# Kernel tuning notes

Hardware: AMD Instinct MI355X
Metric: run time of the kernel (lower is better)

Reference implementation:

```python
import jax, jax.numpy as jnp
import numpy as np

H = 256   # node_hidden_dim == edge_hidden_dim

def _ln(x, g, b):
    m = x.mean(-1, keepdims=True)
    v = ((x - m) ** 2).mean(-1, keepdims=True)
    return (x - m) / jnp.sqrt(v + 1e-5) * g + b

def _slnn(x, W, b, g, beta):
    # Linear -> LayerNorm -> ReLU (SingleLayerNN)
    return jax.nn.relu(_ln(x @ W.T + b, g, beta))

def _gru_mean(x, Wih, Whh, bih, bhh):
    # x: [E, T, Din]; torch GRU gate order (r, z, n); returns mean over time of outputs [E, H]
    h0 = jnp.zeros((x.shape[0], Whh.shape[1]), x.dtype)
    def step(h, xt):
        gi = xt @ Wih.T + bih
        gh = h @ Whh.T + bhh
        ir, iz, inn = jnp.split(gi, 3, axis=-1)
        hr, hz, hn = jnp.split(gh, 3, axis=-1)
        r = jax.nn.sigmoid(ir + hr)
        z = jax.nn.sigmoid(iz + hz)
        n = jnp.tanh(inn + r * hn)
        h_new = (1.0 - z) * n + z * h
        return h_new, h_new
    _, ys = jax.lax.scan(step, h0, jnp.swapaxes(x, 0, 1))  # [T, E, H]
    return ys.mean(axis=0)

def setup_inputs() -> dict:
    key = jax.random.key(0)
    ks = iter(jax.random.split(key, 64))
    rn = lambda shape, s=1.0: (jax.random.normal(next(ks), shape, jnp.float32) * s)
    ru = lambda shape: jax.random.uniform(next(ks), shape, jnp.float32)
    ri = lambda shape, hi: jax.random.randint(next(ks), shape, 0, hi, jnp.int32)
    N0, N1, N2, E0, E1, T = 40000, 10000, 2000, 100000, 20000, 8
    Dn, De, FC, C = 128, 64, 512, 16
    inp = {
        'node_features': rn((N0, Dn)),
        'edge_features_0': rn((E0, T, De)),
        'edge_features_1': rn((E1, T, H)),
        'history_0': rn((N0, H)),
        'history_1': rn((N1, H)),
        'agg_history_1': rn((N2, H)),
        'subg_norm_1': ru((N1, 1)),
        'subg_norm_2': ru((N2, 1)),
        'norm_2': ru((N2, 1)),
        'src0': ri((E0,), N0), 'dst0': ri((E0,), N1),
        'src1': ri((E1,), N1), 'dst1': ri((E1,), N2),
        'self_nid0': ri((N1,), N0), 'self_nid1': ri((N2,), N1),
        # parameters
        'gru0_Wih': rn((3 * H, De), 0.05), 'gru0_Whh': rn((3 * H, H), 0.05),
        'gru0_bih': rn((3 * H,), 0.05), 'gru0_bhh': rn((3 * H,), 0.05),
        'gru1_Wih': rn((3 * H, H), 0.05), 'gru1_Whh': rn((3 * H, H), 0.05),
        'gru1_bih': rn((3 * H,), 0.05), 'gru1_bhh': rn((3 * H,), 0.05),
        'phi0_W': rn((H, Dn + H), 0.05), 'phi0_b': rn((H,), 0.05),
        'phi0_g': jnp.ones((H,)), 'phi0_beta': jnp.zeros((H,)),
        'phi1_W': rn((H, 2 * H), 0.05), 'phi1_b': rn((H,), 0.05),
        'phi1_g': jnp.ones((H,)), 'phi1_beta': jnp.zeros((H,)),
        'nu0_W': rn((H, 2 * H), 0.05), 'nu0_b': rn((H,), 0.05),
        'nu0_g': jnp.ones((H,)), 'nu0_beta': jnp.zeros((H,)),
        'nu1_W': rn((H, 2 * H), 0.05), 'nu1_b': rn((H,), 0.05),
        'nu1_g': jnp.ones((H,)), 'nu1_beta': jnp.zeros((H,)),
        'fc1_W': rn((FC, H), 0.05), 'fc1_b': rn((FC,), 0.05),
        'fc2_W': rn((C, FC), 0.05), 'fc2_b': rn((C,), 0.05),
    }
    return inp

def reference(node_features, edge_features_0, edge_features_1, history_0, history_1,
              agg_history_1, subg_norm_1, subg_norm_2, norm_2,
              gru0_Wih, gru0_Whh, gru0_bih, gru0_bhh,
              gru1_Wih, gru1_Whh, gru1_bih, gru1_bhh,
              phi0_W, phi0_b, phi0_g, phi0_beta,
              phi1_W, phi1_b, phi1_g, phi1_beta,
              nu0_W, nu0_b, nu0_g, nu0_beta,
              nu1_W, nu1_b, nu1_g, nu1_beta,
              fc1_W, fc1_b, fc2_W, fc2_b,
              src0, dst0, src1, dst1, self_nid0, self_nid1):
    N1, N2 = self_nid0.shape[0], self_nid1.shape[0]
    # ---- layer 0 ----
    self_h0 = _slnn(jnp.concatenate([jnp.zeros((N1, H), node_features.dtype),
                                     node_features[self_nid0]], 1),
                    phi0_W, phi0_b, phi0_g, phi0_beta)                       # [N1, H]
    edge_emb0 = _gru_mean(edge_features_0, gru0_Wih, gru0_Whh, gru0_bih, gru0_bhh)  # [E0, H]
    nb0 = _slnn(jnp.concatenate([node_features[src0], edge_emb0], 1),
                phi0_W, phi0_b, phi0_g, phi0_beta)
    msg0 = jax.nn.relu(nb0 - history_0[src0])
    delta_nb0 = jax.ops.segment_sum(msg0, dst0, num_segments=N1)             # scatter-sum
    new_h0 = (delta_nb0 - self_h0) * subg_norm_1
    h1 = _slnn(jnp.concatenate([new_h0, self_h0], 1), nu0_W, nu0_b, nu0_g, nu0_beta)  # [N1, H]
    # ---- layer 1 ----
    self_h1 = _slnn(jnp.concatenate([jnp.zeros((N2, H), h1.dtype), h1[self_nid1]], 1),
                    phi1_W, phi1_b, phi1_g, phi1_beta)                       # [N2, H]
    self_delta_h1 = self_h1 - history_1[self_nid1]
    edge_emb1 = _gru_mean(edge_features_1, gru1_Wih, gru1_Whh, gru1_bih, gru1_bhh)  # [E1, H]
    nb1 = _slnn(jnp.concatenate([h1[src1], edge_emb1], 1),
                phi1_W, phi1_b, phi1_g, phi1_beta)
    msg1 = jax.nn.relu(nb1 - history_1[src1])
    delta_nb1 = jax.ops.segment_sum(msg1, dst1, num_segments=N2)
    new_h1 = (delta_nb1 - self_delta_h1) * subg_norm_2 + agg_history_1 * norm_2
    h2 = _slnn(jnp.concatenate([new_h1, self_h1], 1), nu1_W, nu1_b, nu1_g, nu1_beta)  # [N2, H]
    # ---- readout (no activation between fc1 and fc2, as in source) ----
    logit = (h2 @ fc1_W.T + fc1_b) @ fc2_W.T + fc2_b
    return logit
```

## Files before the change

kernel.cpp:

```cpp
#include <hip/hip_runtime.h>

typedef unsigned short u16;
typedef __attribute__((ext_vector_type(4))) float f32x4;
typedef __attribute__((ext_vector_type(8))) short bf16x8;
#define MFMA16(a,b,c) __builtin_amdgcn_mfma_f32_16x16x32_bf16((a),(b),(c),0,0,0)

template<int N> struct ic { static constexpr int v = N; };

__device__ __forceinline__ u16 f2bf(float f){
  unsigned int u = __float_as_uint(f);
  u += 0x7FFFu + ((u >> 16) & 1u);
  return (u16)(u >> 16);
}
__device__ __forceinline__ float bf2f(u16 h){
  return __uint_as_float(((unsigned int)h) << 16);
}
__device__ __forceinline__ float sigmoid_f(float x){
  x = fminf(fmaxf(x, -30.f), 30.f);
  return __fdividef(1.f, 1.f + __expf(-x));
}
__device__ __forceinline__ float tanh_f(float x){
  x = fminf(fmaxf(x, -15.f), 15.f);
  float e = __expf(-2.f * x);
  return __fdividef(1.f - e, 1.f + e);
}

__global__ void cvt_bf16_kernel(const float* __restrict__ in, u16* __restrict__ out, int n){
  int i = blockIdx.x * 256 + threadIdx.x;
  int stride = gridDim.x * 256;
  for (; i < n; i += stride) out[i] = f2bf(in[i]);
}

template<int R>
__device__ __forceinline__ void ln_stats_rows(const float* __restrict__ O,
                                              float* __restrict__ mean_s,
                                              float* __restrict__ rstd_s){
  const int tid  = threadIdx.x;
  const int wave = tid >> 6, lane = tid & 63;
  constexpr int RW = R / 4;
  #pragma unroll
  for (int rr = 0; rr < RW; rr++){
    const int r = wave * RW + rr;
    float s = 0.f, q = 0.f;
    #pragma unroll
    for (int i = lane; i < 256; i += 64){ float v = O[r*256 + i]; s += v; q += v*v; }
    #pragma unroll
    for (int off = 32; off; off >>= 1){ s += __shfl_down(s, off); q += __shfl_down(q, off); }
    if (lane == 0){
      float m   = s * (1.f/256.f);
      float var = q * (1.f/256.f) - m*m;
      mean_s[r] = m;
      rstd_s[r] = rsqrtf(fmaxf(var, 0.f) + 1e-5f);
    }
  }
}

template<int DIN, int NFD>
__global__ __launch_bounds__(512, 2)
void gru_mfma_kernel(int E,
    const float* __restrict__ x,
    const float* __restrict__ nodef,
    const int*   __restrict__ src,
    const int*   __restrict__ dst,
    const float* __restrict__ hist,
    const u16*   __restrict__ Wih,
    const u16*   __restrict__ Whh,
    const float* __restrict__ bih,
    const float* __restrict__ bhh,
    const u16*   __restrict__ phiW,
    const float* __restrict__ phib,
    const float* __restrict__ phig,
    const float* __restrict__ phibeta,
    float* __restrict__ delta)
{
  constexpr int HP  = 264;
  constexpr int XP  = DIN + 8;
  constexpr int NP  = NFD + 8;
  constexpr int KP  = NFD + 256;
  constexpr int NF4 = DIN / 32;

  __shared__ u16  hb[2 * 64 * HP];
  __shared__ u16  xb[2 * 64 * XP];
  __shared__ float sums_s[8 * 64], sqs_s[8 * 64];
  __shared__ float mean_s[64], rstd_s[64];
  __shared__ int   srcs_s[64], dsts_s[64];

  const int tid  = threadIdx.x;
  const int wave = tid >> 6, lane = tid & 63;
  const int quad = lane >> 4, ln15 = lane & 15;
  const int cbase = wave * 32;
  const int e0   = blockIdx.x * 64;

  if (tid < 64){
    int e  = e0 + tid;
    int ec = (e < E) ? e : (E - 1);
    srcs_s[tid] = src[ec];
    dsts_s[tid] = dst[ec];
  }

  int cn[2]; float brc[2], bzc[2], bnic[2], bnhc[2], pb[2], gg[2], gb[2];
  #pragma unroll
  for (int nt = 0; nt < 2; nt++){
    int c   = cbase + nt * 16 + ln15;
    cn[nt]  = c;
    brc[nt]  = bih[c]       + bhh[c];
    bzc[nt]  = bih[256 + c] + bhh[256 + c];
    bnic[nt] = bih[512 + c];
    bnhc[nt] = bhh[512 + c];
    pb[nt]   = phib[c];
    gg[nt]   = phig[c];
    gb[nt]   = phibeta[c];
  }

  #pragma unroll
  for (int j = 0; j < NF4; j++){
    int i4 = tid + j * 512;
    int e  = i4 / (DIN / 4);
    int k4 = (i4 % (DIN / 4)) * 4;
    int ge = (e0 + e < E) ? (e0 + e) : (E - 1);
    float4 v = *(const float4*)(x + (size_t)ge * (8 * DIN) + k4);
    ushort4 u;
    u.x = f2bf(v.x); u.y = f2bf(v.y); u.z = f2bf(v.z); u.w = f2bf(v.w);
    *(ushort4*)(xb + e * XP + k4) = u;
  }
  __syncthreads();

  float hs[2][4][4];
  #pragma unroll
  for (int nt = 0; nt < 2; nt++)
    #pragma unroll
    for (int mt = 0; mt < 4; mt++)
      #pragma unroll
      for (int q = 0; q < 4; q++) hs[nt][mt][q] = 0.f;

  const f32x4 zero4 = {0.f, 0.f, 0.f, 0.f};

  #pragma unroll 1
  for (int t = 0; t < 8; t++){
    const u16* rd = hb + ((t & 1) ^ 1) * (64 * HP);
    u16*       wr = hb + (t & 1) * (64 * HP);
    const u16* xr = xb + (t & 1) * (64 * XP);

    float4 xpre[NF4];
    if (t < 7){
      #pragma unroll
      for (int j = 0; j < NF4; j++){
        int i4 = tid + j * 512;
        int e  = i4 / (DIN / 4);
        int k4 = (i4 % (DIN / 4)) * 4;
        int ge = (e0 + e < E) ? (e0 + e) : (E - 1);
        xpre[j] = *(const float4*)(x + (size_t)ge * (8 * DIN) + (size_t)(t + 1) * DIN + k4);
      }
    }

    auto phase = [&](auto ntc){
      constexpr int NT = decltype(ntc)::v;
      const int c = cn[NT];
      f32x4 aR[4], aZ[4], aNI[4], aNH[4];
      #pragma unroll
      for (int mt = 0; mt < 4; mt++){
        aR[mt] = zero4; aZ[mt] = zero4; aNI[mt] = zero4; aNH[mt] = zero4;
      }
      if (t > 0){
        #pragma unroll
        for (int kt = 0; kt < 8; kt++){
          bf16x8 a[4];
          #pragma unroll
          for (int mt = 0; mt < 4; mt++)
            a[mt] = *(const bf16x8*)(rd + (mt*16 + ln15) * HP + kt * 32 + quad * 8);
          const u16* bp = Whh + (size_t)c * 256 + kt * 32 + quad * 8;
          bf16x8 br = *(const bf16x8*)(bp);
          bf16x8 bz = *(const bf16x8*)(bp + 256 * 256);
          bf16x8 bn = *(const bf16x8*)(bp + 512 * 256);
          #pragma unroll
          for (int mt = 0; mt < 4; mt++){
            aR[mt]  = MFMA16(a[mt], br, aR[mt]);
            aZ[mt]  = MFMA16(a[mt], bz, aZ[mt]);
            aNH[mt] = MFMA16(a[mt], bn, aNH[mt]);
          }
        }
      }
      #pragma unroll
      for (int kt = 0; kt < DIN / 32; kt++){
        bf16x8 a[4];
        #pragma unroll
        for (int mt = 0; mt < 4; mt++)
          a[mt] = *(const bf16x8*)(xr + (mt*16 + ln15) * XP + kt * 32 + quad * 8);
        const u16* bp = Wih + (size_t)c * DIN + kt * 32 + quad * 8;
        bf16x8 br = *(const bf16x8*)(bp);
        bf16x8 bz = *(const bf16x8*)(bp + 256 * DIN);
        bf16x8 bn = *(const bf16x8*)(bp + 512 * DIN);
        #pragma unroll
        for (int mt = 0; mt < 4; mt++){
          aR[mt]  = MFMA16(a[mt], br, aR[mt]);
          aZ[mt]  = MFMA16(a[mt], bz, aZ[mt]);
          aNI[mt] = MFMA16(a[mt], bn, aNI[mt]);
        }
      }
      #pragma unroll
      for (int mt = 0; mt < 4; mt++){
        #pragma unroll
        for (int q = 0; q < 4; q++){
          const int e = mt * 16 + quad * 4 + q;
          float r = sigmoid_f(aR[mt][q] + brc[NT]);
          float z = sigmoid_f(aZ[mt][q] + bzc[NT]);
          float n = tanh_f(aNI[mt][q] + bnic[NT] + r * (aNH[mt][q] + bnhc[NT]));
          float hold = (t > 0) ? bf2f(rd[e * HP + c]) : 0.f;
          float hnew = (1.f - z) * n + z * hold;
          hs[NT][mt][q] += hnew;
          if (t < 7) wr[e * HP + c] = f2bf(hnew);
        }
      }
    };
    phase(ic<0>());
    phase(ic<1>());

    if (t < 7){
      u16* xw = xb + ((t + 1) & 1) * (64 * XP);
      #pragma unroll
      for (int j = 0; j < NF4; j++){
        int i4 = tid + j * 512;
        int e  = i4 / (DIN / 4);
        int k4 = (i4 % (DIN / 4)) * 4;
        ushort4 u;
        u.x = f2bf(xpre[j].x); u.y = f2bf(xpre[j].y);
        u.z = f2bf(xpre[j].z); u.w = f2bf(xpre[j].w);
        *(ushort4*)(xw + e * XP + k4) = u;
      }
    }
    __syncthreads();
  }

  {
    u16* eb = hb;
    #pragma unroll
    for (int nt = 0; nt < 2; nt++)
      #pragma unroll
      for (int mt = 0; mt < 4; mt++)
        #pragma unroll
        for (int q = 0; q < 4; q++){
          const int e = mt * 16 + quad * 4 + q;
          eb[e * HP + cn[nt]] = f2bf(hs[nt][mt][q] * 0.125f);
        }
    constexpr int R4 = NFD / 4;
    for (int i = tid; i < 64 * R4; i += 512){
      int e  = i / R4;
      int k4 = (i - e * R4) * 4;
      const float4 v = *(const float4*)(nodef + (size_t)srcs_s[e] * NFD + k4);
      ushort4 u;
      u.x = f2bf(v.x); u.y = f2bf(v.y); u.z = f2bf(v.z); u.w = f2bf(v.w);
      *(ushort4*)(xb + e * NP + k4) = u;
    }
  }
  __syncthreads();

  f32x4 P[2][4];
  #pragma unroll
  for (int nt = 0; nt < 2; nt++)
    #pragma unroll
    for (int mt = 0; mt < 4; mt++) P[nt][mt] = zero4;

  #pragma unroll
  for (int kt = 0; kt < NFD / 32; kt++){
    bf16x8 a[4];
    #pragma unroll
    for (int mt = 0; mt < 4; mt++)
      a[mt] = *(const bf16x8*)(xb + (mt*16 + ln15) * NP + kt * 32 + quad * 8);
    #pragma unroll
    for (int nt = 0; nt < 2; nt++){
      const u16* bp = phiW + (size_t)cn[nt] * KP + kt * 32 + quad * 8;
      bf16x8 b = *(const bf16x8*)(bp);
      #pragma unroll
      for (int mt = 0; mt < 4; mt++) P[nt][mt] = MFMA16(a[mt], b, P[nt][mt]);
    }
  }
  #pragma unroll
  for (int kt = 0; kt < 8; kt++){
    bf16x8 a[4];
    #pragma unroll
    for (int mt = 0; mt < 4; mt++)
      a[mt] = *(const bf16x8*)(hb + (mt*16 + ln15) * HP + kt * 32 + quad * 8);
    #pragma unroll
    for (int nt = 0; nt < 2; nt++){
      const u16* bp = phiW + (size_t)cn[nt] * KP + NFD + kt * 32 + quad * 8;
      bf16x8 b = *(const bf16x8*)(bp);
      #pragma unroll
      for (int mt = 0; mt < 4; mt++) P[nt][mt] = MFMA16(a[mt], b, P[nt][mt]);
    }
  }

  float sl[4][4], sq_[4][4];
  #pragma unroll
  for (int mt = 0; mt < 4; mt++)
    #pragma unroll
    for (int q = 0; q < 4; q++){
      float v0 = P[0][mt][q] + pb[0];
      float v1 = P[1][mt][q] + pb[1];
      P[0][mt][q] = v0; P[1][mt][q] = v1;
      sl[mt][q]  = v0 + v1;
      sq_[mt][q] = v0 * v0 + v1 * v1;
    }
  #pragma unroll
  for (int off = 1; off < 16; off <<= 1){
    #pragma unroll
    for (int mt = 0; mt < 4; mt++)
      #pragma unroll
      for (int q = 0; q < 4; q++){
        sl[mt][q]  += __shfl_xor(sl[mt][q], off);
        sq_[mt][q] += __shfl_xor(sq_[mt][q], off);
      }
  }
  if (ln15 == 0){
    #pragma unroll
    for (int mt = 0; mt < 4; mt++)
      #pragma unroll
      for (int q = 0; q < 4; q++){
        int row = mt * 16 + quad * 4 + q;
        sums_s[wave * 64 + row] = sl[mt][q];
        sqs_s[wave * 64 + row]  = sq_[mt][q];
      }
  }
  __syncthreads();
  if (tid < 64){
    float m = 0.f, qq = 0.f;
    #pragma unroll
    for (int w = 0; w < 8; w++){ m += sums_s[w * 64 + tid]; qq += sqs_s[w * 64 + tid]; }
    m  *= (1.f / 256.f);
    qq *= (1.f / 256.f);
    mean_s[tid] = m;
    rstd_s[tid] = rsqrtf(fmaxf(qq - m * m, 0.f) + 1e-5f);
  }
  __syncthreads();

  #pragma unroll
  for (int nt = 0; nt < 2; nt++){
    const int c = cn[nt];
    #pragma unroll
    for (int mt = 0; mt < 4; mt++)
      #pragma unroll
      for (int q = 0; q < 4; q++){
        const int e  = mt * 16 + quad * 4 + q;
        const int ge = e0 + e;
        float y = (P[nt][mt][q] - mean_s[e]) * rstd_s[e] * gg[nt] + gb[nt];
        y = fmaxf(y, 0.f);
        float mv = y - hist[(size_t)srcs_s[e] * 256 + c];
        if (ge < E && mv > 0.f)
          atomicAdd(delta + (size_t)dsts_s[e] * 256 + c, mv);
      }
  }
}

template<int K, int WS>
__global__ __launch_bounds__(256)
void self_slnn_kernel(int N,
    const float* __restrict__ feat,
    const int*   __restrict__ nid,
    const float* __restrict__ W,
    const float* __restrict__ b,
    const float* __restrict__ g,
    const float* __restrict__ beta,
    const float* __restrict__ hist,
    float* __restrict__ out,
    float* __restrict__ out2)
{
  constexpr int R = 8;
  __shared__ float X[R*K];
  __shared__ float O[R*256];
  __shared__ float mean_s[R], rstd_s[R];
  __shared__ int   nids[R];
  const int tid = threadIdx.x;
  const int n0  = blockIdx.x * R;
  if (tid < R) nids[tid] = (n0 + tid < N) ? nid[n0 + tid] : 0;
  __syncthreads();
  for (int i = tid; i < R*K; i += 256){
    int r = i / K, k = i - r*K;
    X[i] = feat[(size_t)nids[r]*K + k];
  }
  __syncthreads();
  const int c = tid;
  const float* Wc = W + (size_t)c*WS + (WS - K);
  float acc[R];
  const float bc0 = b[c];
  #pragma unroll
  for (int r = 0; r < R; r++) acc[r] = bc0;
  #pragma unroll 1
  for (int k = 0; k < K; k += 4){
    float4 w = *(const float4*)(Wc + k);
    #pragma unroll
    for (int r = 0; r < R; r++){
      float4 xv = *(const float4*)(X + r*K + k);
      acc[r] += w.x*xv.x + w.y*xv.y + w.z*xv.z + w.w*xv.w;
    }
  }
  #pragma unroll
  for (int r = 0; r < R; r++) O[r*256 + c] = acc[r];
  __syncthreads();
  ln_stats_rows<R>(O, mean_s, rstd_s);
  __syncthreads();
  const float gc = g[c], bc = beta[c];
  #pragma unroll
  for (int r = 0; r < R; r++){
    int n = n0 + r;
    if (n < N){
      float y = fmaxf((acc[r] - mean_s[r]) * rstd_s[r] * gc + bc, 0.f);
      out[(size_t)n*256 + c] = y;
      if (out2) out2[(size_t)n*256 + c] = y - hist[(size_t)nids[r]*256 + c];
    }
  }
}

__global__ __launch_bounds__(256)
void compose_slnn_kernel(int N,
    const float* __restrict__ delta,
    const float* __restrict__ selfA,
    const float* __restrict__ selfB,
    const float* __restrict__ subg,
    const float* __restrict__ agg,
    const float* __restrict__ normv,
    const float* __restrict__ W,
    const float* __restrict__ b,
    const float* __restrict__ g,
    const float* __restrict__ beta,
    float* __restrict__ out)
{
  constexpr int R = 8;
  __shared__ float X[R*512];
  __shared__ float O[R*256];
  __shared__ float mean_s[R], rstd_s[R];
  const int tid = threadIdx.x;
  const int n0  = blockIdx.x * R;
  for (int i = tid; i < R*512; i += 256){
    int r = i >> 9, k = i & 511;
    int n = n0 + r;
    float v = 0.f;
    if (n < N){
      if (k < 256){
        v = (delta[(size_t)n*256 + k] - selfA[(size_t)n*256 + k]) * subg[n];
        if (agg) v += agg[(size_t)n*256 + k] * normv[n];
      } else {
        v = selfB[(size_t)n*256 + (k - 256)];
      }
    }
    X[i] = v;
  }
  __syncthreads();
  const int c = tid;
  const float* Wc = W + (size_t)c*512;
  float acc[R];
  const float bc0 = b[c];
  #pragma unroll
  for (int r = 0; r < R; r++) acc[r] = bc0;
  #pragma unroll 1
  for (int k = 0; k < 512; k += 4){
    float4 w = *(const float4*)(Wc + k);
    #pragma unroll
    for (int r = 0; r < R; r++){
      float4 xv = *(const float4*)(X + r*512 + k);
      acc[r] += w.x*xv.x + w.y*xv.y + w.z*xv.z + w.w*xv.w;
    }
  }
  #pragma unroll
  for (int r = 0; r < R; r++) O[r*256 + c] = acc[r];
  __syncthreads();
  ln_stats_rows<R>(O, mean_s, rstd_s);
  __syncthreads();
  const float gc = g[c], bc = beta[c];
  #pragma unroll
  for (int r = 0; r < R; r++){
    int n = n0 + r;
    if (n < N)
      out[(size_t)n*256 + c] = fmaxf((acc[r] - mean_s[r]) * rstd_s[r] * gc + bc, 0.f);
  }
}

__global__ __launch_bounds__(256)
void readout_kernel(int N,
    const float* __restrict__ h2,
    const float* __restrict__ W1,
    const float* __restrict__ b1,
    const float* __restrict__ W2,
    const float* __restrict__ b2,
    float* __restrict__ out)
{
  constexpr int R = 8;
  __shared__ float X[R*256];
  __shared__ float T[R*512];
  const int tid = threadIdx.x;
  const int n0  = blockIdx.x * R;
  for (int i = tid; i < R*256; i += 256){
    int r = i >> 8, k = i & 255;
    int n = n0 + r;
    X[i] = (n < N) ? h2[(size_t)n*256 + k] : 0.f;
  }
  __syncthreads();
  const int c = tid;
  const float* Wa = W1 + (size_t)c*256;
  const float* Wb = W1 + (size_t)(c+256)*256;
  float acca[R], accb[R];
  const float ba = b1[c], bb = b1[c+256];
  #pragma unroll
  for (int r = 0; r < R; r++){ acca[r] = ba; accb[r] = bb; }
  #pragma unroll 1
  for (int k = 0; k < 256; k += 4){
    float4 wa = *(const float4*)(Wa + k);
    float4 wb = *(const float4*)(Wb + k);
    #pragma unroll
    for (int r = 0; r < R; r++){
      float4 xv = *(const float4*)(X + r*256 + k);
      acca[r] += wa.x*xv.x + wa.y*xv.y + wa.z*xv.z + wa.w*xv.w;
      accb[r] += wb.x*xv.x + wb.y*xv.y + wb.z*xv.z + wb.w*xv.w;
    }
  }
  #pragma unroll
  for (int r = 0; r < R; r++){ T[r*512 + c] = acca[r]; T[r*512 + 256 + c] = accb[r]; }
  __syncthreads();
  if (tid < R*16){
    int r = tid >> 4, o = tid & 15;
    int n = n0 + r;
    if (n < N){
      float s = b2[o];
      const float* w  = W2 + (size_t)o*512;
      const float* tr = T + r*512;
      #pragma unroll 4
      for (int k = 0; k < 512; k++) s += tr[k]*w[k];
      out[(size_t)n*16 + o] = s;
    }
  }
}

extern "C" void kernel_launch(void* const* d_in, const int* in_sizes, int n_in,
                              void* d_out, int out_size, void* d_ws, size_t ws_size,
                              hipStream_t stream) {
  const float* nf     = (const float*)d_in[0];
  const float* x0     = (const float*)d_in[1];
  const float* x1     = (const float*)d_in[2];
  const float* hist0  = (const float*)d_in[3];
  const float* hist1  = (const float*)d_in[4];
  const float* aggh1  = (const float*)d_in[5];
  const float* subg1  = (const float*)d_in[6];
  const float* subg2  = (const float*)d_in[7];
  const float* norm2  = (const float*)d_in[8];
  const int*   src0   = (const int*)d_in[9];
  const int*   dst0   = (const int*)d_in[10];
  const int*   src1   = (const int*)d_in[11];
  const int*   dst1   = (const int*)d_in[12];
  const int*   nid0   = (const int*)d_in[13];
  const int*   nid1   = (const int*)d_in[14];
  const float* g0Wih  = (const float*)d_in[15];
  const float* g0Whh  = (const float*)d_in[16];
  const float* g0bih  = (const float*)d_in[17];
  const float* g0bhh  = (const float*)d_in[18];
  const float* g1Wih  = (const float*)d_in[19];
  const float* g1Whh  = (const float*)d_in[20];
  const float* g1bih  = (const float*)d_in[21];
  const float* g1bhh  = (const float*)d_in[22];
  const float* phi0W  = (const float*)d_in[23];
  const float* phi0b  = (const float*)d_in[24];
  const float* phi0g  = (const float*)d_in[25];
  const float* phi0be = (const float*)d_in[26];
  const float* phi1W  = (const float*)d_in[27];
  const float* phi1b  = (const float*)d_in[28];
  const float* phi1g  = (const float*)d_in[29];
  const float* phi1be = (const float*)d_in[30];
  const float* nu0W   = (const float*)d_in[31];
  const float* nu0b   = (const float*)d_in[32];
  const float* nu0g   = (const float*)d_in[33];
  const float* nu0be  = (const float*)d_in[34];
  const float* nu1W   = (const float*)d_in[35];
  const float* nu1b   = (const float*)d_in[36];
  const float* nu1g   = (const float*)d_in[37];
  const float* nu1be  = (const float*)d_in[38];
  const float* fc1W   = (const float*)d_in[39];
  const float* fc1b   = (const float*)d_in[40];
  const float* fc2W   = (const float*)d_in[41];
  const float* fc2b   = (const float*)d_in[42];

  const int E0 = in_sizes[9];
  const int E1 = in_sizes[11];
  const int N1 = in_sizes[13];
  const int N2 = in_sizes[14];

  float* ws     = (float*)d_ws;
  float* delta0 = ws;
  float* selfh0 = delta0 + (size_t)N1*256;
  float* h1p    = selfh0 + (size_t)N1*256;
  float* delta1 = h1p    + (size_t)N1*256;
  float* selfh1 = delta1 + (size_t)N2*256;
  float* selfd1 = selfh1 + (size_t)N2*256;
  float* h2p    = selfd1 + (size_t)N2*256;

  u16* wbf       = (u16*)(h2p + (size_t)N2*256);
  u16* g0Wih_bf  = wbf;
  u16* g0Whh_bf  = g0Wih_bf + 768*64;
  u16* phi0W_bf  = g0Whh_bf + 768*256;
  u16* g1Wih_bf  = phi0W_bf + 256*384;
  u16* g1Whh_bf  = g1Wih_bf + 768*256;
  u16* phi1W_bf  = g1Whh_bf + 768*256;

  hipMemsetAsync(delta0, 0, (size_t)N1*256*sizeof(float), stream);
  hipMemsetAsync(delta1, 0, (size_t)N2*256*sizeof(float), stream);

  cvt_bf16_kernel<<<192, 256, 0, stream>>>(g0Wih, g0Wih_bf, 768*64);
  cvt_bf16_kernel<<<768, 256, 0, stream>>>(g0Whh, g0Whh_bf, 768*256);
  cvt_bf16_kernel<<<384, 256, 0, stream>>>(phi0W, phi0W_bf, 256*384);
  cvt_bf16_kernel<<<768, 256, 0, stream>>>(g1Wih, g1Wih_bf, 768*256);
  cvt_bf16_kernel<<<768, 256, 0, stream>>>(g1Whh, g1Whh_bf, 768*256);
  cvt_bf16_kernel<<<512, 256, 0, stream>>>(phi1W, phi1W_bf, 256*512);

  const int gN1 = (N1 + 7) / 8;
  const int gN2 = (N2 + 7) / 8;

  self_slnn_kernel<128, 384><<<gN1, 256, 0, stream>>>(
      N1, nf, nid0, phi0W, phi0b, phi0g, phi0be, nullptr, selfh0, nullptr);

  gru_mfma_kernel<64, 128><<<(E0 + 63) / 64, 512, 0, stream>>>(
      E0, x0, nf, src0, dst0, hist0,
      g0Wih_bf, g0Whh_bf, g0bih, g0bhh,
      phi0W_bf, phi0b, phi0g, phi0be, delta0);

  compose_slnn_kernel<<<gN1, 256, 0, stream>>>(
      N1, delta0, selfh0, selfh0, subg1, nullptr, nullptr,
      nu0W, nu0b, nu0g, nu0be, h1p);

  self_slnn_kernel<256, 512><<<gN2, 256, 0, stream>>>(
      N2, h1p, nid1, phi1W, phi1b, phi1g, phi1be, hist1, selfh1, selfd1);

  gru_mfma_kernel<256, 256><<<(E1 + 63) / 64, 512, 0, stream>>>(
      E1, x1, h1p, src1, dst1, hist1,
      g1Wih_bf, g1Whh_bf, g1bih, g1bhh,
      phi1W_bf, phi1b, phi1g, phi1be, delta1);

  compose_slnn_kernel<<<gN2, 256, 0, stream>>>(
      N2, delta1, selfd1, selfh1, subg2, aggh1, norm2,
      nu1W, nu1b, nu1g, nu1be, h2p);

  readout_kernel<<<gN2, 256, 0, stream>>>(
      N2, h2p, fc1W, fc1b, fc2W, fc2b, (float*)d_out);

  (void)n_in; (void)out_size; (void)ws_size;
}
```

Baseline: 2.812 ms.

## Template GRU kernel on edge tile size and x buffering to raise occupancy

The GRU+phi kernel is templated on edge tile rows (TM) and the number of x staging buffers. Layer 0 keeps 64-edge tiles but uses a single x buffer with an extra barrier. Layer 1 uses 32-edge tiles with double buffering. LayerNorm scratch now aliases freed shared buffers, and launch bounds go from 2 to 4 blocks per CU. This cuts LDS use and register pressure so more blocks stay resident and the layer-1 grid has more blocks. The cost is extra synchronisation, lower MFMA reuse per weight load in layer 1, and possible register spills under the tighter bound.

```diff
diff --git a/kernel.cpp b/kernel.cpp
--- a/kernel.cpp
+++ b/kernel.cpp
@@ -55,8 +55,8 @@
   }
 }
 
-template<int DIN, int NFD>
-__global__ __launch_bounds__(512, 2)
+template<int TM, int DIN, int NFD, int XBUFS>
+__global__ __launch_bounds__(512, 4)
 void gru_mfma_kernel(int E,
     const float* __restrict__ x,
     const float* __restrict__ nodef,
@@ -73,25 +73,27 @@
     const float* __restrict__ phibeta,
     float* __restrict__ delta)
 {
-  constexpr int HP  = 264;
-  constexpr int XP  = DIN + 8;
-  constexpr int NP  = NFD + 8;
-  constexpr int KP  = NFD + 256;
-  constexpr int NF4 = DIN / 32;
-
-  __shared__ u16  hb[2 * 64 * HP];
-  __shared__ u16  xb[2 * 64 * XP];
-  __shared__ float sums_s[8 * 64], sqs_s[8 * 64];
-  __shared__ float mean_s[64], rstd_s[64];
-  __shared__ int   srcs_s[64], dsts_s[64];
+  constexpr int HP   = 264;
+  constexpr int XP   = DIN + 8;
+  constexpr int NP   = NFD + 8;
+  constexpr int KP   = NFD + 256;
+  constexpr int MT   = TM / 16;
+  constexpr int NF4  = (TM * DIN) / 2048;
+  constexpr int HBUF = TM * HP;
+  constexpr int XBUF = TM * XP;
+
+  __shared__ __align__(16) u16 hb[2 * HBUF];
+  __shared__ __align__(16) u16 xb[XBUFS * XBUF];
+  __shared__ int srcs_s[TM], dsts_s[TM];
 
   const int tid  = threadIdx.x;
   const int wave = tid >> 6, lane = tid & 63;
   const int quad = lane >> 4, ln15 = lane & 15;
+  const int qoff = quad * 8;
   const int cbase = wave * 32;
-  const int e0   = blockIdx.x * 64;
-
-  if (tid < 64){
+  const int e0   = blockIdx.x * TM;
+
+  if (tid < TM){
     int e  = e0 + tid;
     int ec = (e < E) ? e : (E - 1);
     srcs_s[tid] = src[ec];
@@ -125,11 +127,11 @@
   }
   __syncthreads();
 
-  float hs[2][4][4];
+  float hs[2][MT][4];
   #pragma unroll
   for (int nt = 0; nt < 2; nt++)
     #pragma unroll
-    for (int mt = 0; mt < 4; mt++)
+    for (int mt = 0; mt < MT; mt++)
       #pragma unroll
       for (int q = 0; q < 4; q++) hs[nt][mt][q] = 0.f;
 
@@ -137,9 +139,9 @@
 
   #pragma unroll 1
   for (int t = 0; t < 8; t++){
-    const u16* rd = hb + ((t & 1) ^ 1) * (64 * HP);
-    u16*       wr = hb + (t & 1) * (64 * HP);
-    const u16* xr = xb + (t & 1) * (64 * XP);
+    const u16* rd = hb + ((t & 1) ^ 1) * HBUF;
+    u16*       wr = hb + (t & 1) * HBUF;
+    const u16* xr = xb + ((XBUFS == 2) ? (t & 1) * XBUF : 0);
 
     float4 xpre[NF4];
     if (t < 7){
@@ -156,24 +158,24 @@
     auto phase = [&](auto ntc){
       constexpr int NT = decltype(ntc)::v;
       const int c = cn[NT];
-      f32x4 aR[4], aZ[4], aNI[4], aNH[4];
-      #pragma unroll
-      for (int mt = 0; mt < 4; mt++){
+      f32x4 aR[MT], aZ[MT], aNI[MT], aNH[MT];
+      #pragma unroll
+      for (int mt = 0; mt < MT; mt++){
         aR[mt] = zero4; aZ[mt] = zero4; aNI[mt] = zero4; aNH[mt] = zero4;
       }
       if (t > 0){
         #pragma unroll
         for (int kt = 0; kt < 8; kt++){
-          bf16x8 a[4];
+          bf16x8 a[MT];
           #pragma unroll
-          for (int mt = 0; mt < 4; mt++)
-            a[mt] = *(const bf16x8*)(rd + (mt*16 + ln15) * HP + kt * 32 + quad * 8);
-          const u16* bp = Whh + (size_t)c * 256 + kt * 32 + quad * 8;
+          for (int mt = 0; mt < MT; mt++)
+            a[mt] = *(const bf16x8*)(rd + (mt*16 + ln15) * HP + kt * 32 + qoff);
+          const u16* bp = Whh + (size_t)c * 256 + kt * 32 + qoff;
           bf16x8 br = *(const bf16x8*)(bp);
           bf16x8 bz = *(const bf16x8*)(bp + 256 * 256);
           bf16x8 bn = *(const bf16x8*)(bp + 512 * 256);
           #pragma unroll
-          for (int mt = 0; mt < 4; mt++){
+          for (int mt = 0; mt < MT; mt++){
             aR[mt]  = MFMA16(a[mt], br, aR[mt]);
             aZ[mt]  = MFMA16(a[mt], bz, aZ[mt]);
             aNH[mt] = MFMA16(a[mt], bn, aNH[mt]);
@@ -182,23 +184,23 @@
       }
       #pragma unroll
       for (int kt = 0; kt < DIN / 32; kt++){
-        bf16x8 a[4];
+        bf16x8 a[MT];
         #pragma unroll
-        for (int mt = 0; mt < 4; mt++)
-          a[mt] = *(const bf16x8*)(xr + (mt*16 + ln15) * XP + kt * 32 + quad * 8);
-        const u16* bp = Wih + (size_t)c * DIN + kt * 32 + quad * 8;
+        for (int mt = 0; mt < MT; mt++)
+          a[mt] = *(const bf16x8*)(xr + (mt*16 + ln15) * XP + kt * 32 + qoff);
+        const u16* bp = Wih + (size_t)c * DIN + kt * 32 + qoff;
         bf16x8 br = *(const bf16x8*)(bp);
         bf16x8 bz = *(const bf16x8*)(bp + 256 * DIN);
         bf16x8 bn = *(const bf16x8*)(bp + 512 * DIN);
         #pragma unroll
-        for (int mt = 0; mt < 4; mt++){
+        for (int mt = 0; mt < MT; mt++){
           aR[mt]  = MFMA16(a[mt], br, aR[mt]);
           aZ[mt]  = MFMA16(a[mt], bz, aZ[mt]);
           aNI[mt] = MFMA16(a[mt], bn, aNI[mt]);
         }
       }
       #pragma unroll
-      for (int mt = 0; mt < 4; mt++){
+      for (int mt = 0; mt < MT; mt++){
         #pragma unroll
         for (int q = 0; q < 4; q++){
           const int e = mt * 16 + quad * 4 + q;
@@ -215,83 +217,106 @@
     phase(ic<0>());
     phase(ic<1>());
 
-    if (t < 7){
-      u16* xw = xb + ((t + 1) & 1) * (64 * XP);
-      #pragma unroll
-      for (int j = 0; j < NF4; j++){
-        int i4 = tid + j * 512;
-        int e  = i4 / (DIN / 4);
-        int k4 = (i4 % (DIN / 4)) * 4;
-        ushort4 u;
-        u.x = f2bf(xpre[j].x); u.y = f2bf(xpre[j].y);
-        u.z = f2bf(xpre[j].z); u.w = f2bf(xpre[j].w);
-        *(ushort4*)(xw + e * XP + k4) = u;
-      }
-    }
-    __syncthreads();
-  }
-
+    if (XBUFS == 1){
+      __syncthreads();
+      if (t < 7){
+        #pragma unroll
+        for (int j = 0; j < NF4; j++){
+          int i4 = tid + j * 512;
+          int e  = i4 / (DIN / 4);
+          int k4 = (i4 % (DIN / 4)) * 4;
+          ushort4 u;
+          u.x = f2bf(xpre[j].x); u.y = f2bf(xpre[j].y);
+          u.z = f2bf(xpre[j].z); u.w = f2bf(xpre[j].w);
+          *(ushort4*)(xb + e * XP + k4) = u;
+        }
+        __syncthreads();
+      }
+    } else {
+      if (t < 7){
+        u16* xw = xb + (((t + 1) & 1)) * XBUF;
+        #pragma unroll
+        for (int j = 0; j < NF4; j++){
+          int i4 = tid + j * 512;
+          int e  = i4 / (DIN / 4);
+          int k4 = (i4 % (DIN / 4)) * 4;
+          ushort4 u;
+          u.x = f2bf(xpre[j].x); u.y = f2bf(xpre[j].y);
+          u.z = f2bf(xpre[j].z); u.w = f2bf(xpre[j].w);
+          *(ushort4*)(xw + e * XP + k4) = u;
+        }
+      }
+      __syncthreads();
+    }
+  }
+
+  u16* nb = (XBUFS == 1) ? (hb + HBUF) : xb;
   {
     u16* eb = hb;
     #pragma unroll
     for (int nt = 0; nt < 2; nt++)
       #pragma unroll
-      for (int mt = 0; mt < 4; mt++)
+      for (int mt = 0; mt < MT; mt++)
         #pragma unroll
         for (int q = 0; q < 4; q++){
           const int e = mt * 16 + quad * 4 + q;
           eb[e * HP + cn[nt]] = f2bf(hs[nt][mt][q] * 0.125f);
         }
     constexpr int R4 = NFD / 4;
-    for (int i = tid; i < 64 * R4; i += 512){
+    for (int i = tid; i < TM * R4; i += 512){
       int e  = i / R4;
       int k4 = (i - e * R4) * 4;
       const float4 v = *(const float4*)(nodef + (size_t)srcs_s[e] * NFD + k4);
       ushort4 u;
       u.x = f2bf(v.x); u.y = f2bf(v.y); u.z = f2bf(v.z); u.w = f2bf(v.w);
-      *(ushort4*)(xb + e * NP + k4) = u;
-    }
-  }
-  __syncthreads();
-
-  f32x4 P[2][4];
+      *(ushort4*)(nb + e * NP + k4) = u;
+    }
+  }
+  __syncthreads();
+
+  f32x4 P[2][MT];
   #pragma unroll
   for (int nt = 0; nt < 2; nt++)
     #pragma unroll
-    for (int mt = 0; mt < 4; mt++) P[nt][mt] = zero4;
+    for (int mt = 0; mt < MT; mt++) P[nt][mt] = zero4;
 
   #pragma unroll
   for (int kt = 0; kt < NFD / 32; kt++){
-    bf16x8 a[4];
-    #pragma unroll
-    for (int mt = 0; mt < 4; mt++)
-      a[mt] = *(const bf16x8*)(xb + (mt*16 + ln15) * NP + kt * 32 + quad * 8);
+    bf16x8 a[MT];
+    #pragma unroll
+    for (int mt = 0; mt < MT; mt++)
+      a[mt] = *(const bf16x8*)(nb + (mt*16 + ln15) * NP + kt * 32 + qoff);
     #pragma unroll
     for (int nt = 0; nt < 2; nt++){
-      const u16* bp = phiW + (size_t)cn[nt] * KP + kt * 32 + quad * 8;
+      const u16* bp = phiW + (size_t)cn[nt] * KP + kt * 32 + qoff;
       bf16x8 b = *(const bf16x8*)(bp);
       #pragma unroll
-      for (int mt = 0; mt < 4; mt++) P[nt][mt] = MFMA16(a[mt], b, P[nt][mt]);
+      for (int mt = 0; mt < MT; mt++) P[nt][mt] = MFMA16(a[mt], b, P[nt][mt]);
     }
   }
   #pragma unroll
   for (int kt = 0; kt < 8; kt++){
-    bf16x8 a[4];
-    #pragma unroll
-    for (int mt = 0; mt < 4; mt++)
-      a[mt] = *(const bf16x8*)(hb + (mt*16 + ln15) * HP + kt * 32 + quad * 8);
+    bf16x8 a[MT];
+    #pragma unroll
+    for (int mt = 0; mt < MT; mt++)
+      a[mt] = *(const bf16x8*)(hb + (mt*16 + ln15) * HP + kt * 32 + qoff);
     #pragma unroll
     for (int nt = 0; nt < 2; nt++){
-      const u16* bp = phiW + (size_t)cn[nt] * KP + NFD + kt * 32 + quad * 8;
+      const u16* bp = phiW + (size_t)cn[nt] * KP + NFD + kt * 32 + qoff;
       bf16x8 b = *(const bf16x8*)(bp);
       #pragma unroll
-      for (int mt = 0; mt < 4; mt++) P[nt][mt] = MFMA16(a[mt], b, P[nt][mt]);
-    }
-  }
-
-  float sl[4][4], sq_[4][4];
-  #pragma unroll
-  for (int mt = 0; mt < 4; mt++)
+      for (int mt = 0; mt < MT; mt++) P[nt][mt] = MFMA16(a[mt], b, P[nt][mt]);
+    }
+  }
+
+  float* sums_s = (float*)((XBUFS == 1) ? (void*)xb : (void*)(hb + HBUF));
+  float* sqs_s  = sums_s + 8 * TM;
+  float* mean_s = sqs_s  + 8 * TM;
+  float* rstd_s = mean_s + TM;
+
+  float sl[MT][4], sq_[MT][4];
+  #pragma unroll
+  for (int mt = 0; mt < MT; mt++)
     #pragma unroll
     for (int q = 0; q < 4; q++){
       float v0 = P[0][mt][q] + pb[0];
@@ -303,7 +328,7 @@
   #pragma unroll
   for (int off = 1; off < 16; off <<= 1){
     #pragma unroll
-    for (int mt = 0; mt < 4; mt++)
+    for (int mt = 0; mt < MT; mt++)
       #pragma unroll
       for (int q = 0; q < 4; q++){
         sl[mt][q]  += __shfl_xor(sl[mt][q], off);
@@ -312,19 +337,19 @@
   }
   if (ln15 == 0){
     #pragma unroll
-    for (int mt = 0; mt < 4; mt++)
+    for (int mt = 0; mt < MT; mt++)
       #pragma unroll
       for (int q = 0; q < 4; q++){
         int row = mt * 16 + quad * 4 + q;
-        sums_s[wave * 64 + row] = sl[mt][q];
-        sqs_s[wave * 64 + row]  = sq_[mt][q];
-      }
-  }
-  __syncthreads();
-  if (tid < 64){
+        sums_s[wave * TM + row] = sl[mt][q];
+        sqs_s[wave * TM + row]  = sq_[mt][q];
+      }
+  }
+  __syncthreads();
+  if (tid < TM){
     float m = 0.f, qq = 0.f;
     #pragma unroll
-    for (int w = 0; w < 8; w++){ m += sums_s[w * 64 + tid]; qq += sqs_s[w * 64 + tid]; }
+    for (int w = 0; w < 8; w++){ m += sums_s[w * TM + tid]; qq += sqs_s[w * TM + tid]; }
     m  *= (1.f / 256.f);
     qq *= (1.f / 256.f);
     mean_s[tid] = m;
@@ -336,7 +361,7 @@
   for (int nt = 0; nt < 2; nt++){
     const int c = cn[nt];
     #pragma unroll
-    for (int mt = 0; mt < 4; mt++)
+    for (int mt = 0; mt < MT; mt++)
       #pragma unroll
       for (int q = 0; q < 4; q++){
         const int e  = mt * 16 + quad * 4 + q;
@@ -613,7 +638,7 @@
   self_slnn_kernel<128, 384><<<gN1, 256, 0, stream>>>(
       N1, nf, nid0, phi0W, phi0b, phi0g, phi0be, nullptr, selfh0, nullptr);
 
-  gru_mfma_kernel<64, 128><<<(E0 + 63) / 64, 512, 0, stream>>>(
+  gru_mfma_kernel<64, 64, 128, 1><<<(E0 + 63) / 64, 512, 0, stream>>>(
       E0, x0, nf, src0, dst0, hist0,
       g0Wih_bf, g0Whh_bf, g0bih, g0bhh,
       phi0W_bf, phi0b, phi0g, phi0be, delta0);
@@ -625,7 +650,7 @@
   self_slnn_kernel<256, 512><<<gN2, 256, 0, stream>>>(
       N2, h1p, nid1, phi1W, phi1b, phi1g, phi1be, hist1, selfh1, selfd1);
 
-  gru_mfma_kernel<256, 256><<<(E1 + 63) / 64, 512, 0, stream>>>(
+  gru_mfma_kernel<32, 256, 256, 2><<<(E1 + 31) / 32, 512, 0, stream>>>(
       E1, x1, h1p, src1, dst1, hist1,
       g1Wih_bf, g1Whh_bf, g1bih, g1bhh,
       phi1W_bf, phi1b, phi1g, phi1be, delta1);
```

New measurement: 4.001 ms. 1.42x slower.
